# Optimization experiments

Measured on AMD Instinct MI355X. Metric: run time of the kernel, lower is better.

The kernel has to match this reference:

```python
import jax, jax.numpy as jnp
import numpy as np
from jax import lax

B, N, E = 256, 100_000, 3_200_000
VOCAB, EMB, FT, DIM, OUT = 65, 128, 41, 32, 128
BN_EPS = 1e-5


def setup_inputs() -> dict:
    key = jax.random.key(0)
    ks = jax.random.split(key, 40)
    f = lambda i, shape: jax.random.normal(ks[i], shape, jnp.float32) * 0.05
    inp = {
        'xd': jax.random.randint(ks[0], (B, 100), 0, VOCAB),
        'xt': jax.random.normal(ks[1], (N, FT), jnp.float32),
        'edge_index': jax.random.randint(ks[2], (2, E), 0, N),
        'batch': jnp.sort(jax.random.randint(ks[3], (N,), 0, B)),
        'y': jax.random.normal(ks[4], (B,), jnp.float32),
        # drug branch params
        'emb': f(5, (VOCAB, EMB)),
        'conv_w': f(6, (32, 100, 8)),   # OIH for Conv1d(100->32, k=8)
        'conv_b': f(7, (32,)),
        'fcd_w': f(8, (32 * 121, OUT)),
        'fcd_b': f(9, (OUT,)),
        # GIN layer 1 MLP (41->32->32)
        'g1_w1': f(10, (FT, DIM)), 'g1_b1': f(11, (DIM,)),
        'g1_w2': f(12, (DIM, DIM)), 'g1_b2': f(13, (DIM,)),
        # GIN layers 2-5 MLPs (32->32->32), stacked
        'gw1': f(14, (4, DIM, DIM)), 'gb1': f(15, (4, DIM)),
        'gw2': f(16, (4, DIM, DIM)), 'gb2': f(17, (4, DIM)),
        # BatchNorm (eval mode running stats) for 5 layers
        'bn_g': f(18, (5, DIM)) + 1.0,
        'bn_b': f(19, (5, DIM)),
        'bn_rm': f(20, (5, DIM)),
        'bn_rv': jax.random.uniform(ks[21], (5, DIM), jnp.float32, 0.5, 1.5),
        # protein fc + classifier
        'fct_w': f(22, (DIM, OUT)), 'fct_b': f(23, (OUT,)),
        'c1_w': f(24, (256, 1024)), 'c1_b': f(25, (1024,)),
        'c2_w': f(26, (1024, 256)), 'c2_b': f(27, (256,)),
        'c3_w': f(28, (256, 1)), 'c3_b': f(29, (1,)),
    }
    return inp


def reference(xd, xt, edge_index, batch, y, emb, conv_w, conv_b, fcd_w, fcd_b,
              g1_w1, g1_b1, g1_w2, g1_b2, gw1, gb1, gw2, gb2,
              bn_g, bn_b, bn_rm, bn_rv, fct_w, fct_b,
              c1_w, c1_b, c2_w, c2_b, c3_w, c3_b):
    # ---- drug branch ----
    e = emb[xd]                                        # [B, 100, 128]
    c = lax.conv_general_dilated(e, conv_w, (1,), 'VALID',
                                 dimension_numbers=('NCH', 'OIH', 'NCH'))
    c = c + conv_b[None, :, None]                      # [B, 32, 121]
    xd_f = c.reshape(B, 32 * 121) @ fcd_w + fcd_b      # [B, 128]

    src, dst = edge_index[0], edge_index[1]
    h = xt
    for i in range(5):
        agg = h + jax.ops.segment_sum(h[src], dst, num_segments=N)
        if i == 0:
            w1, b1, w2, b2 = g1_w1, g1_b1, g1_w2, g1_b2
        else:
            w1, b1, w2, b2 = gw1[i - 1], gb1[i - 1], gw2[i - 1], gb2[i - 1]
        h = jax.nn.relu(agg @ w1 + b1) @ w2 + b2       # GIN MLP
        h = jax.nn.relu(h)                              # F.relu after conv
        h = bn_g[i] * (h - bn_rm[i]) * lax.rsqrt(bn_rv[i] + BN_EPS) + bn_b[i]
    pooled = jax.ops.segment_sum(h, batch, num_segments=B)  # global_add_pool
    xt_f = jax.nn.relu(pooled @ fct_w + fct_b)         # dropout = identity (eval)

    # ---- classifier ----
    xj = jnp.concatenate([xd_f, xt_f], axis=1)         # [B, 256]
    h1 = jax.nn.relu(xj @ c1_w + c1_b)
    h2 = jax.nn.relu(h1 @ c2_w + c2_b)
    out = (h2 @ c3_w + c3_b).squeeze(1)                # [B]
    return out, y
```

## Files before the change

kernel.cpp:

```cpp
#include <hip/hip_runtime.h>

typedef unsigned int u32;

#define NN 100000
#define NE 3200000
#define NB 256
#define FTD 41
#define DIM 32
#define NBK 782
#define SCHUNK 8000

__global__ __launch_bounds__(256) void k_bzero(int* __restrict__ bcnt) {
  int g = blockIdx.x * 256 + threadIdx.x;
  if (g < NBK) bcnt[g] = 0;
}

__global__ __launch_bounds__(256) void k_bhist(const int* __restrict__ ei,
                                               int* __restrict__ bcnt) {
  __shared__ int h[NBK];
  int t = threadIdx.x;
  for (int i = t; i < NBK; i += 256) h[i] = 0;
  __syncthreads();
  for (int g = blockIdx.x * 256 + t; g < NE; g += gridDim.x * 256)
    atomicAdd(&h[ei[NE + g] >> 7], 1);
  __syncthreads();
  for (int i = t; i < NBK; i += 256)
    if (h[i]) atomicAdd(&bcnt[i], h[i]);
}

__global__ __launch_bounds__(1024) void k_bscan(const int* __restrict__ bcnt,
                                                int* __restrict__ boff,
                                                int* __restrict__ bcur) {
  __shared__ int sm[1024];
  int t = threadIdx.x;
  int v = (t < NBK) ? bcnt[t] : 0;
  sm[t] = v;
  __syncthreads();
  for (int d = 1; d < 1024; d <<= 1) {
    int x = (t >= d) ? sm[t - d] : 0;
    __syncthreads();
    sm[t] += x;
    __syncthreads();
  }
  if (t < NBK) {
    int excl = sm[t] - v;
    boff[t] = excl;
    bcur[t] = excl;
  }
  if (t == 0) boff[NBK] = NE;
}

__global__ __launch_bounds__(256) void k_bscatter(const int* __restrict__ ei,
                                                  int* __restrict__ bcur,
                                                  int* __restrict__ ppack) {
  __shared__ int lexcl[NBK];
  __shared__ int lcur[NBK];
  __shared__ int gdelta[NBK];
  __shared__ int lbuf[SCHUNK];
  __shared__ unsigned short lbkt[SCHUNK];
  __shared__ int sm[256];
  int t = threadIdx.x;
  int e0 = blockIdx.x * SCHUNK;
  for (int i = t; i < NBK; i += 256) lexcl[i] = 0;
  __syncthreads();
  for (int i = t; i < SCHUNK; i += 256)
    atomicAdd(&lexcl[((u32)ei[NE + e0 + i]) >> 7], 1);
  __syncthreads();
  int b0 = t * 4;
  int c0 = 0, c1 = 0, c2 = 0, c3 = 0;
  if (b0 < NBK) {
    c0 = lexcl[b0];
    c1 = (b0 + 1 < NBK) ? lexcl[b0 + 1] : 0;
    c2 = (b0 + 2 < NBK) ? lexcl[b0 + 2] : 0;
    c3 = (b0 + 3 < NBK) ? lexcl[b0 + 3] : 0;
  }
  int tot = c0 + c1 + c2 + c3;
  sm[t] = tot;
  __syncthreads();
  for (int d = 1; d < 256; d <<= 1) {
    int x = (t >= d) ? sm[t - d] : 0;
    __syncthreads();
    sm[t] += x;
    __syncthreads();
  }
  int base = sm[t] - tot;
  if (b0 < NBK) {
    int cnts[4] = {c0, c1, c2, c3};
    int e = base;
#pragma unroll
    for (int j = 0; j < 4; j++) {
      int b = b0 + j;
      if (b < NBK) {
        int c = cnts[j];
        lexcl[b] = e;
        lcur[b] = e;
        if (c > 0) gdelta[b] = atomicAdd(&bcur[b], c) - e;
        e += c;
      }
    }
  }
  __syncthreads();
  for (int i = t; i < SCHUNK; i += 256) {
    int s = ei[e0 + i];
    u32 d = (u32)ei[NE + e0 + i];
    int b = d >> 7;
    int p = atomicAdd(&lcur[b], 1);
    lbuf[p] = (int)(((d & 127u) << 20) | (u32)s);
    lbkt[p] = (unsigned short)b;
  }
  __syncthreads();
  for (int i = t; i < SCHUNK; i += 256) {
    int b = lbkt[i];
    ppack[gdelta[b] + i] = lbuf[i];
  }
}

__global__ __launch_bounds__(256) void k_bfinal(const int* __restrict__ boff,
                                                const int* __restrict__ ppack,
                                                int* __restrict__ off,
                                                int* __restrict__ srcs) {
  __shared__ int ncnt[128];
  __shared__ int nincl[128];
  int b = blockIdx.x, t = threadIdx.x;
  int e0 = boff[b], e1 = boff[b + 1];
  if (t < 128) ncnt[t] = 0;
  __syncthreads();
  for (int i = e0 + t; i < e1; i += 256) atomicAdd(&ncnt[((u32)ppack[i]) >> 20], 1);
  __syncthreads();
  if (t < 128) nincl[t] = ncnt[t];
  __syncthreads();
  for (int d = 1; d < 128; d <<= 1) {
    int x = 0;
    if (t < 128 && t >= d) x = nincl[t - d];
    __syncthreads();
    if (t < 128) nincl[t] += x;
    __syncthreads();
  }
  int node0 = b * 128;
  if (t < 128) {
    int excl = nincl[t] - ncnt[t];
    int node = node0 + t;
    if (node < NN) off[node] = e0 + excl;
    ncnt[t] = excl;
  }
  if (b == 0 && t == 0) off[NN] = NE;
  __syncthreads();
  for (int i = e0 + t; i < e1; i += 256) {
    u32 v = (u32)ppack[i];
    int dl = v >> 20;
    int pos = atomicAdd(&ncnt[dl], 1);
    srcs[e0 + pos] = (int)(v & 0xFFFFF);
  }
}

__global__ __launch_bounds__(256) void k_conv(
    const int* __restrict__ xd, const float* __restrict__ emb,
    const float* __restrict__ convw, const float* __restrict__ convb,
    float* __restrict__ C) {
  __shared__ float e_s[100 * 128];
  __shared__ float w_s[4 * 800];
  __shared__ int xd_s[100];
  int t = threadIdx.x;
  int b = blockIdx.x >> 3;
  int og = (blockIdx.x & 7) << 2;
  if (t < 100) xd_s[t] = xd[b * 100 + t];
  __syncthreads();
  for (int i = t; i < 12800; i += 256)
    e_s[i] = emb[xd_s[i >> 7] * 128 + (i & 127)];
  for (int i = t; i < 3200; i += 256) w_s[i] = convw[og * 800 + i];
  __syncthreads();
  for (int idx = t; idx < 484; idx += 256) {
    int o = idx / 121, h = idx - o * 121;
    const float* wp = &w_s[o * 800];
    const float* ep = &e_s[h];
    float acc = 0.f;
    for (int i = 0; i < 100; i++) {
#pragma unroll
      for (int k = 0; k < 8; k++) acc += ep[i * 128 + k] * wp[i * 8 + k];
    }
    C[b * 3872 + (og + o) * 121 + h] = acc + convb[og + o];
  }
}

__global__ __launch_bounds__(256) void k_fcd(
    const float* __restrict__ C, const float* __restrict__ fcdw,
    const float* __restrict__ fcdb, float* __restrict__ XJ) {
  __shared__ float c_s[3872];
  __shared__ float red[128];
  int t = threadIdx.x, b = blockIdx.x;
  for (int i = t; i < 3872; i += 256) c_s[i] = C[b * 3872 + i];
  __syncthreads();
  int j = t & 127, half = t >> 7;
  float acc = 0.f;
  int k0 = half * 1936;
  for (int k = k0; k < k0 + 1936; k++) acc += c_s[k] * fcdw[k * 128 + j];
  if (half) red[j] = acc;
  __syncthreads();
  if (!half) XJ[b * 256 + j] = acc + red[j] + fcdb[j];
}

__global__ __launch_bounds__(256) void k_z1(
    const float* __restrict__ xt, const float* __restrict__ w1,
    float* __restrict__ Z, float* __restrict__ pool) {
  __shared__ float xs[256 * FTD];
  __shared__ float w1s[FTD * DIM];
  int t = threadIdx.x;
  int base = blockIdx.x * 256;
  int g = base + t;
  if (g < NB * DIM) pool[g] = 0.f;
  for (int i = t; i < FTD * DIM; i += 256) w1s[i] = w1[i];
  int cnt = min(256, NN - base);
  for (int i = t; i < cnt * FTD; i += 256) xs[i] = xt[base * FTD + i];
  __syncthreads();
  int n = base + t;
  if (n < NN) {
    float acc[DIM];
#pragma unroll
    for (int j = 0; j < DIM; j++) acc[j] = 0.f;
    for (int k = 0; k < FTD; k++) {
      float xk = xs[t * FTD + k];
#pragma unroll
      for (int j = 0; j < DIM; j++) acc[j] += xk * w1s[k * DIM + j];
    }
    float* zp = &Z[n * DIM];
#pragma unroll
    for (int j = 0; j < DIM; j++) zp[j] = acc[j];
  }
}

template <int HAS_NEXT, int DO_POOL>
__global__ __launch_bounds__(256) void k_gin(
    const int* __restrict__ off, const int* __restrict__ srcs,
    const float* __restrict__ Zin, const float* __restrict__ b1,
    const float* __restrict__ w2, const float* __restrict__ b2,
    const float* __restrict__ bng, const float* __restrict__ bnb,
    const float* __restrict__ bnrm, const float* __restrict__ bnrv,
    const float* __restrict__ w1n, float* __restrict__ Zout,
    float* __restrict__ pool, const int* __restrict__ batch) {
  int t = threadIdx.x;
  int f = t & 31;
  int n = blockIdx.x * 8 + (t >> 5);
  int beg = off[n], end = off[n + 1];
  float a0 = Zin[n * DIM + f], a1 = 0.f, a2 = 0.f, a3 = 0.f;
  for (int base = beg; base < end; base += 32) {
    int idx = base + f;
    int sv = (idx < end) ? srcs[idx] : -1;
#pragma unroll
    for (int k = 0; k < 32; k += 4) {
      int s0 = __shfl(sv, k, 32);
      int s1 = __shfl(sv, k + 1, 32);
      int s2 = __shfl(sv, k + 2, 32);
      int s3 = __shfl(sv, k + 3, 32);
      float v0 = Zin[max(s0, 0) * DIM + f];
      float v1 = Zin[max(s1, 0) * DIM + f];
      float v2 = Zin[max(s2, 0) * DIM + f];
      float v3 = Zin[max(s3, 0) * DIM + f];
      a0 += (s0 >= 0) ? v0 : 0.f;
      a1 += (s1 >= 0) ? v1 : 0.f;
      a2 += (s2 >= 0) ? v2 : 0.f;
      a3 += (s3 >= 0) ? v3 : 0.f;
    }
  }
  float acc = (a0 + a1) + (a2 + a3);
  float hid = fmaxf(acc + b1[f], 0.f);
  float o = b2[f];
#pragma unroll
  for (int k = 0; k < DIM; k++) o += __shfl(hid, k, 32) * w2[k * DIM + f];
  float sc = bng[f] * rsqrtf(bnrv[f] + 1e-5f);
  float hn = fmaxf(o, 0.f) * sc + (bnb[f] - bnrm[f] * sc);
  if (HAS_NEXT) {
    float z = 0.f;
#pragma unroll
    for (int k = 0; k < DIM; k++) z += __shfl(hn, k, 32) * w1n[k * DIM + f];
    Zout[n * DIM + f] = z;
  }
  if (DO_POOL) atomicAdd(&pool[batch[n] * DIM + f], hn);
}

__global__ __launch_bounds__(128) void k_fct(
    const float* __restrict__ pool, const float* __restrict__ fctw,
    const float* __restrict__ fctb, float* __restrict__ XJ) {
  __shared__ float p_s[DIM];
  int t = threadIdx.x, b = blockIdx.x;
  if (t < DIM) p_s[t] = pool[b * DIM + t];
  __syncthreads();
  float acc = fctb[t];
  for (int k = 0; k < DIM; k++) acc += p_s[k] * fctw[k * 128 + t];
  XJ[b * 256 + 128 + t] = fmaxf(acc, 0.f);
}

__global__ __launch_bounds__(256) void k_c1(
    const float* __restrict__ XJ, const float* __restrict__ w,
    const float* __restrict__ bias, float* __restrict__ H1) {
  __shared__ float xs[256];
  int t = threadIdx.x, b = blockIdx.y;
  xs[t] = XJ[b * 256 + t];
  __syncthreads();
  int j = blockIdx.x * 256 + t;
  float acc = bias[j];
  for (int k = 0; k < 256; k++) acc += xs[k] * w[k * 1024 + j];
  H1[b * 1024 + j] = fmaxf(acc, 0.f);
}

__global__ __launch_bounds__(256) void k_c2(
    const float* __restrict__ H1, const float* __restrict__ w,
    const float* __restrict__ bias, float* __restrict__ H2) {
  __shared__ float hs[1024];
  int t = threadIdx.x, b = blockIdx.x;
  for (int i = t; i < 1024; i += 256) hs[i] = H1[b * 1024 + i];
  __syncthreads();
  float acc = bias[t];
  for (int k = 0; k < 1024; k++) acc += hs[k] * w[k * 256 + t];
  H2[b * 256 + t] = fmaxf(acc, 0.f);
}

__global__ __launch_bounds__(64) void k_c3(
    const float* __restrict__ H2, const float* __restrict__ w,
    const float* __restrict__ bias, const float* __restrict__ y,
    float* __restrict__ out) {
  int b = blockIdx.x * 64 + threadIdx.x;
  float acc = bias[0];
  for (int k = 0; k < 256; k++) acc += H2[b * 256 + k] * w[k];
  out[b] = acc;
  out[NB + b] = y[b];
}

extern "C" void kernel_launch(void* const* d_in, const int* in_sizes, int n_in,
                              void* d_out, int out_size, void* d_ws,
                              size_t ws_size, hipStream_t stream) {
  const int* xd = (const int*)d_in[0];
  const float* xt = (const float*)d_in[1];
  const int* ei = (const int*)d_in[2];
  const int* batch = (const int*)d_in[3];
  const float* y = (const float*)d_in[4];
  const float* emb = (const float*)d_in[5];
  const float* convw = (const float*)d_in[6];
  const float* convb = (const float*)d_in[7];
  const float* fcdw = (const float*)d_in[8];
  const float* fcdb = (const float*)d_in[9];
  const float* g1w1 = (const float*)d_in[10];
  const float* g1b1 = (const float*)d_in[11];
  const float* g1w2 = (const float*)d_in[12];
  const float* g1b2 = (const float*)d_in[13];
  const float* gw1 = (const float*)d_in[14];
  const float* gb1 = (const float*)d_in[15];
  const float* gw2 = (const float*)d_in[16];
  const float* gb2 = (const float*)d_in[17];
  const float* bng = (const float*)d_in[18];
  const float* bnb = (const float*)d_in[19];
  const float* bnrm = (const float*)d_in[20];
  const float* bnrv = (const float*)d_in[21];
  const float* fctw = (const float*)d_in[22];
  const float* fctb = (const float*)d_in[23];
  const float* c1w = (const float*)d_in[24];
  const float* c1b = (const float*)d_in[25];
  const float* c2w = (const float*)d_in[26];
  const float* c2b = (const float*)d_in[27];
  const float* c3w = (const float*)d_in[28];
  const float* c3b = (const float*)d_in[29];
  float* out = (float*)d_out;

  float* ws = (float*)d_ws;
  float* Z0 = ws;
  float* Z1 = Z0 + (size_t)NN * DIM;
  int* srcs = (int*)(Z1 + (size_t)NN * DIM);
  int* off = srcs + NE;
  int* bcnt = off + NN + 1;
  int* boff = bcnt + NBK;
  int* bcur = boff + NBK + 1;
  int* ppack = bcur + NBK;
  float* C = (float*)ppack;
  float* XJ = C + (size_t)NB * 3872;
  float* H1 = XJ + NB * 256;
  float* H2 = H1 + NB * 1024;
  float* POOL = H2 + NB * 256;

  int nblk = (NN + 255) / 256;

  k_bzero<<<(NBK + 255) / 256, 256, 0, stream>>>(bcnt);
  k_bhist<<<512, 256, 0, stream>>>(ei, bcnt);
  k_bscan<<<1, 1024, 0, stream>>>(bcnt, boff, bcur);
  k_bscatter<<<NE / SCHUNK, 256, 0, stream>>>(ei, bcur, ppack);
  k_bfinal<<<NBK, 256, 0, stream>>>(boff, ppack, off, srcs);

  k_conv<<<NB * 8, 256, 0, stream>>>(xd, emb, convw, convb, C);
  k_fcd<<<NB, 256, 0, stream>>>(C, fcdw, fcdb, XJ);

  k_z1<<<nblk, 256, 0, stream>>>(xt, g1w1, Z0, POOL);
  float* zin = Z0;
  float* zout = Z1;
  for (int i = 0; i < 5; i++) {
    const float *b1, *w2, *b2;
    if (i == 0) { b1 = g1b1; w2 = g1w2; b2 = g1b2; }
    else {
      b1 = gb1 + (i - 1) * DIM;
      w2 = gw2 + (i - 1) * DIM * DIM;
      b2 = gb2 + (i - 1) * DIM;
    }
    const float* w1n = gw1 + i * DIM * DIM;
    if (i < 4)
      k_gin<1, 0><<<NN / 8, 256, 0, stream>>>(
          off, srcs, zin, b1, w2, b2, bng + i * DIM, bnb + i * DIM,
          bnrm + i * DIM, bnrv + i * DIM, w1n, zout, POOL, batch);
    else
      k_gin<0, 1><<<NN / 8, 256, 0, stream>>>(
          off, srcs, zin, b1, w2, b2, bng + i * DIM, bnb + i * DIM,
          bnrm + i * DIM, bnrv + i * DIM, w1n, zout, POOL, batch);
    float* tmp = zin; zin = zout; zout = tmp;
  }
  k_fct<<<NB, 128, 0, stream>>>(POOL, fctw, fctb, XJ);
  k_c1<<<dim3(4, NB), 256, 0, stream>>>(XJ, c1w, c1b, H1);
  k_c2<<<NB, 256, 0, stream>>>(H1, c2w, c2b, H2);
  k_c3<<<4, 64, 0, stream>>>(H2, c3w, c3b, y, out);
}
```

Baseline: 810.1 us.

## Store GIN node features in fp16 and process multiple nodes per warp

```diff
diff --git a/kernel.cpp b/kernel.cpp
--- a/kernel.cpp
+++ b/kernel.cpp
@@ -1,6 +1,7 @@
 #include <hip/hip_runtime.h>
 
 typedef unsigned int u32;
+typedef _Float16 f16;
 
 #define NN 100000
 #define NE 3200000
@@ -9,6 +10,7 @@
 #define DIM 32
 #define NBK 782
 #define SCHUNK 8000
+#define NPB 16
 
 __global__ __launch_bounds__(256) void k_bzero(int* __restrict__ bcnt) {
   int g = blockIdx.x * 256 + threadIdx.x;
@@ -201,7 +203,7 @@
 
 __global__ __launch_bounds__(256) void k_z1(
     const float* __restrict__ xt, const float* __restrict__ w1,
-    float* __restrict__ Z, float* __restrict__ pool) {
+    f16* __restrict__ Z, float* __restrict__ pool) {
   __shared__ float xs[256 * FTD];
   __shared__ float w1s[FTD * DIM];
   int t = threadIdx.x;
@@ -222,59 +224,80 @@
 #pragma unroll
       for (int j = 0; j < DIM; j++) acc[j] += xk * w1s[k * DIM + j];
     }
-    float* zp = &Z[n * DIM];
-#pragma unroll
-    for (int j = 0; j < DIM; j++) zp[j] = acc[j];
+    f16* zp = &Z[(size_t)n * DIM];
+#pragma unroll
+    for (int j = 0; j < DIM; j++) zp[j] = (f16)acc[j];
   }
 }
 
 template <int HAS_NEXT, int DO_POOL>
 __global__ __launch_bounds__(256) void k_gin(
     const int* __restrict__ off, const int* __restrict__ srcs,
-    const float* __restrict__ Zin, const float* __restrict__ b1,
+    const f16* __restrict__ Zin, const float* __restrict__ b1,
     const float* __restrict__ w2, const float* __restrict__ b2,
     const float* __restrict__ bng, const float* __restrict__ bnb,
     const float* __restrict__ bnrm, const float* __restrict__ bnrv,
-    const float* __restrict__ w1n, float* __restrict__ Zout,
+    const float* __restrict__ w1n, f16* __restrict__ Zout,
     float* __restrict__ pool, const int* __restrict__ batch) {
-  int t = threadIdx.x;
+  __shared__ float w2s[DIM * DIM];
+  __shared__ float w1ns[DIM * DIM];
+  int t = threadIdx.x;
+  for (int i = t; i < DIM * DIM; i += 256) {
+    w2s[i] = w2[i];
+    if (HAS_NEXT) w1ns[i] = w1n[i];
+  }
   int f = t & 31;
-  int n = blockIdx.x * 8 + (t >> 5);
-  int beg = off[n], end = off[n + 1];
-  float a0 = Zin[n * DIM + f], a1 = 0.f, a2 = 0.f, a3 = 0.f;
-  for (int base = beg; base < end; base += 32) {
-    int idx = base + f;
-    int sv = (idx < end) ? srcs[idx] : -1;
-#pragma unroll
-    for (int k = 0; k < 32; k += 4) {
-      int s0 = __shfl(sv, k, 32);
-      int s1 = __shfl(sv, k + 1, 32);
-      int s2 = __shfl(sv, k + 2, 32);
-      int s3 = __shfl(sv, k + 3, 32);
-      float v0 = Zin[max(s0, 0) * DIM + f];
-      float v1 = Zin[max(s1, 0) * DIM + f];
-      float v2 = Zin[max(s2, 0) * DIM + f];
-      float v3 = Zin[max(s3, 0) * DIM + f];
-      a0 += (s0 >= 0) ? v0 : 0.f;
-      a1 += (s1 >= 0) ? v1 : 0.f;
-      a2 += (s2 >= 0) ? v2 : 0.f;
-      a3 += (s3 >= 0) ? v3 : 0.f;
-    }
-  }
-  float acc = (a0 + a1) + (a2 + a3);
-  float hid = fmaxf(acc + b1[f], 0.f);
-  float o = b2[f];
-#pragma unroll
-  for (int k = 0; k < DIM; k++) o += __shfl(hid, k, 32) * w2[k * DIM + f];
+  float b1f = b1[f], b2f = b2[f];
   float sc = bng[f] * rsqrtf(bnrv[f] + 1e-5f);
-  float hn = fmaxf(o, 0.f) * sc + (bnb[f] - bnrm[f] * sc);
-  if (HAS_NEXT) {
-    float z = 0.f;
-#pragma unroll
-    for (int k = 0; k < DIM; k++) z += __shfl(hn, k, 32) * w1n[k * DIM + f];
-    Zout[n * DIM + f] = z;
-  }
-  if (DO_POOL) atomicAdd(&pool[batch[n] * DIM + f], hn);
+  float sh = bnb[f] - bnrm[f] * sc;
+  __syncthreads();
+  int n0 = blockIdx.x * NPB + (t >> 5) * (NPB / 8);
+  for (int n = n0; n < n0 + NPB / 8; n++) {
+    int beg = off[n], end = off[n + 1];
+    float a0 = (float)Zin[(size_t)n * DIM + f];
+    float a1 = 0.f, a2 = 0.f, a3 = 0.f, a4 = 0.f, a5 = 0.f, a6 = 0.f, a7 = 0.f;
+    for (int base = beg; base < end; base += 32) {
+      int idx = base + f;
+      int sv = (idx < end) ? __builtin_nontemporal_load(&srcs[idx]) : 0;
+      int m = min(32, end - base);
+      int k = 0;
+      for (; k + 8 <= m; k += 8) {
+        int s0 = __shfl(sv, k, 32);
+        int s1 = __shfl(sv, k + 1, 32);
+        int s2 = __shfl(sv, k + 2, 32);
+        int s3 = __shfl(sv, k + 3, 32);
+        int s4 = __shfl(sv, k + 4, 32);
+        int s5 = __shfl(sv, k + 5, 32);
+        int s6 = __shfl(sv, k + 6, 32);
+        int s7 = __shfl(sv, k + 7, 32);
+        a0 += (float)Zin[s0 * DIM + f];
+        a1 += (float)Zin[s1 * DIM + f];
+        a2 += (float)Zin[s2 * DIM + f];
+        a3 += (float)Zin[s3 * DIM + f];
+        a4 += (float)Zin[s4 * DIM + f];
+        a5 += (float)Zin[s5 * DIM + f];
+        a6 += (float)Zin[s6 * DIM + f];
+        a7 += (float)Zin[s7 * DIM + f];
+      }
+      for (; k < m; k++) {
+        int s = __shfl(sv, k, 32);
+        a0 += (float)Zin[s * DIM + f];
+      }
+    }
+    float acc = ((a0 + a1) + (a2 + a3)) + ((a4 + a5) + (a6 + a7));
+    float hid = fmaxf(acc + b1f, 0.f);
+    float o = b2f;
+#pragma unroll
+    for (int k = 0; k < DIM; k++) o += __shfl(hid, k, 32) * w2s[k * DIM + f];
+    float hn = fmaxf(o, 0.f) * sc + sh;
+    if (HAS_NEXT) {
+      float z = 0.f;
+#pragma unroll
+      for (int k = 0; k < DIM; k++) z += __shfl(hn, k, 32) * w1ns[k * DIM + f];
+      __builtin_nontemporal_store((f16)z, &Zout[(size_t)n * DIM + f]);
+    }
+    if (DO_POOL) atomicAdd(&pool[batch[n] * DIM + f], hn);
+  }
 }
 
 __global__ __launch_bounds__(128) void k_fct(
@@ -361,8 +384,8 @@
   float* out = (float*)d_out;
 
   float* ws = (float*)d_ws;
-  float* Z0 = ws;
-  float* Z1 = Z0 + (size_t)NN * DIM;
+  f16* Z0 = (f16*)ws;
+  f16* Z1 = Z0 + (size_t)NN * DIM;
   int* srcs = (int*)(Z1 + (size_t)NN * DIM);
   int* off = srcs + NE;
   int* bcnt = off + NN + 1;
@@ -387,8 +410,8 @@
   k_fcd<<<NB, 256, 0, stream>>>(C, fcdw, fcdb, XJ);
 
   k_z1<<<nblk, 256, 0, stream>>>(xt, g1w1, Z0, POOL);
-  float* zin = Z0;
-  float* zout = Z1;
+  f16* zin = Z0;
+  f16* zout = Z1;
   for (int i = 0; i < 5; i++) {
     const float *b1, *w2, *b2;
     if (i == 0) { b1 = g1b1; w2 = g1w2; b2 = g1b2; }
@@ -399,14 +422,14 @@
     }
     const float* w1n = gw1 + i * DIM * DIM;
     if (i < 4)
-      k_gin<1, 0><<<NN / 8, 256, 0, stream>>>(
+      k_gin<1, 0><<<NN / NPB, 256, 0, stream>>>(
           off, srcs, zin, b1, w2, b2, bng + i * DIM, bnb + i * DIM,
           bnrm + i * DIM, bnrv + i * DIM, w1n, zout, POOL, batch);
     else
-      k_gin<0, 1><<<NN / 8, 256, 0, stream>>>(
+      k_gin<0, 1><<<NN / NPB, 256, 0, stream>>>(
           off, srcs, zin, b1, w2, b2, bng + i * DIM, bnb + i * DIM,
           bnrm + i * DIM, bnrv + i * DIM, w1n, zout, POOL, batch);
-    float* tmp = zin; zin = zout; zout = tmp;
+    f16* tmp = zin; zin = zout; zout = tmp;
   }
   k_fct<<<NB, 128, 0, stream>>>(POOL, fctw, fctb, XJ);
   k_c1<<<dim3(4, NB), 256, 0, stream>>>(XJ, c1w, c1b, H1);
```

Measured after the change: 1.056 ms. 1.3x slower.
